# Kernel tuning notes

Measured on AMD Instinct MI355X. Metric: run time of the kernel, lower is better.

Reference implementation:

```python
import jax, jax.numpy as jnp
import numpy as np

NUM_USERS = 100_000
NUM_ITEMS = 50_000
N = NUM_USERS + NUM_ITEMS
E_DIR = 600_000            # directed user->item interactions
E = 2 * E_DIR              # bidirectional edge list used by LGConv
D = 64                     # embed_dim
F_EDGE = 8                 # edge_mlp_input_dim (edge_attr 7 + edge_weight_init 1)
H_MLP = 32                 # edge_mlp_hidden_dim
NUM_ARTISTS = 20_000
NUM_ALBUMS = 40_000
NUM_LAYERS = 3
AUDIO_SCALE = 0.3
META_SCALE = 0.44


def l2norm(x, eps=1e-12):
    # matches torch F.normalize(p=2, dim=-1)
    n = jnp.linalg.norm(x, axis=-1, keepdims=True)
    return x / jnp.maximum(n, eps)


def setup_inputs() -> dict:
    key = jax.random.key(0)
    ks = jax.random.split(key, 12)
    u = jax.random.randint(ks[0], (E_DIR,), 0, NUM_USERS)
    it = jax.random.randint(ks[1], (E_DIR,), 0, NUM_ITEMS) + NUM_USERS
    # bidirectional edges over the concatenated [user; item] node space
    edge_index = jnp.stack([jnp.concatenate([u, it]), jnp.concatenate([it, u])], axis=0)
    return {
        'user_emb_w': 0.01 * jax.random.normal(ks[2], (NUM_USERS, D), jnp.float32),
        'item_audio_emb': jax.random.normal(ks[3], (NUM_ITEMS, D), jnp.float32),
        'artist_emb_w': jax.random.normal(ks[4], (NUM_ARTISTS, D), jnp.float32) * (6.0 / (NUM_ARTISTS + D)) ** 0.5,
        'album_emb_w': jax.random.normal(ks[5], (NUM_ALBUMS, D), jnp.float32) * (6.0 / (NUM_ALBUMS + D)) ** 0.5,
        'mlp_w1': jax.random.normal(ks[6], (F_EDGE, H_MLP), jnp.float32) * (1.0 / F_EDGE) ** 0.5,
        'mlp_b1': jnp.zeros((H_MLP,), jnp.float32),
        'mlp_w2': jax.random.normal(ks[7], (H_MLP, 1), jnp.float32) * (1.0 / H_MLP) ** 0.5,
        'mlp_b2': jnp.zeros((1,), jnp.float32),
        'edge_features': jax.random.uniform(ks[8], (E, F_EDGE), jnp.float32),
        'edge_index': edge_index,
        'artist_ids': jax.random.randint(ks[9], (NUM_ITEMS,), 0, NUM_ARTISTS),
        'album_ids': jax.random.randint(ks[10], (NUM_ITEMS,), 0, NUM_ALBUMS),
    }


def reference(user_emb_w, item_audio_emb, artist_emb_w, album_emb_w,
              mlp_w1, mlp_b1, mlp_w2, mlp_b2, edge_features,
              edge_index, artist_ids, album_ids):
    # Edge weight MLP: Linear -> ReLU -> Linear -> Sigmoid -> squeeze
    h = jax.nn.relu(edge_features @ mlp_w1 + mlp_b1)
    edge_w = jax.nn.sigmoid(h @ mlp_w2 + mlp_b2)[:, 0]  # [E]

    # Node features
    user = l2norm(user_emb_w)
    meta = artist_emb_w[artist_ids] + album_emb_w[album_ids]
    item = l2norm(item_audio_emb * AUDIO_SCALE + meta * META_SCALE)
    x = jnp.concatenate([user, item], axis=0)  # [N, D]

    row, col = edge_index[0], edge_index[1]

    # gcn_norm (add_self_loops=False): deg over destination column
    deg = jax.ops.segment_sum(edge_w, col, num_segments=N)
    dinv = jnp.where(deg > 0, 1.0 / jnp.sqrt(jnp.where(deg > 0, deg, 1.0)), 0.0)
    norm = dinv[row] * edge_w * dinv[col]  # [E]

    acc = x
    for _ in range(NUM_LAYERS):
        msg = norm[:, None] * x[row]                         # gather [E, D]
        x = jax.ops.segment_sum(msg, col, num_segments=N)    # scatter-add
        acc = acc + x
    x = l2norm(acc / (NUM_LAYERS + 1))

    user_emb = x[:NUM_USERS]
    item_emb = x[NUM_USERS:]
    align_loss = jnp.float32(0.0)
    return user_emb, item_emb, align_loss
```

## Files before the change

### kernel.cpp

```cpp
#include <hip/hip_runtime.h>
#include <math.h>

#define NUM_USERS 100000
#define NUM_ITEMS 50000
#define NN 150000
#define EE 1200000
#define NNP 150016
#define G8_BLOCKS 4688

#define NBUCKET 293
#define NB2 256
#define EPB 4688

typedef unsigned short ushort_t;
typedef unsigned int uint_t;

__device__ __forceinline__ uint_t pack2(float lo, float hi) {
    uint_t a = __float_as_uint(lo);
    uint_t b = __float_as_uint(hi);
    a = (a + 0x7FFFu + ((a >> 16) & 1u)) >> 16;
    b = (b + 0x7FFFu + ((b >> 16) & 1u)) & 0xFFFF0000u;
    return a | b;
}
__device__ __forceinline__ float lo16(uint_t x) { return __uint_as_float(x << 16); }
__device__ __forceinline__ float hi16(uint_t x) { return __uint_as_float(x & 0xFFFF0000u); }

__global__ void mlp_kernel(const float* __restrict__ feats,
                           const float* __restrict__ w1,
                           const float* __restrict__ b1,
                           const float* __restrict__ w2,
                           const float* __restrict__ b2,
                           float* __restrict__ wout) {
    __shared__ float sw1t[256];
    __shared__ float2 shb[32];
    __shared__ float sb2s;
    int t = threadIdx.x;
    sw1t[t] = w1[(t & 7) * 32 + (t >> 3)];
    if (t < 32) shb[t] = make_float2(b1[t], w2[t]);
    if (t == 0) sb2s = b2[0];
    __syncthreads();
    int e = blockIdx.x * 256 + t;
    if (e >= EE) return;
    const float4* fp = (const float4*)(feats + (size_t)e * 8);
    float4 fa = fp[0], fb = fp[1];
    float f[8] = {fa.x, fa.y, fa.z, fa.w, fb.x, fb.y, fb.z, fb.w};
    float s = sb2s;
#pragma unroll
    for (int j = 0; j < 32; ++j) {
        float4 wa = *(const float4*)&sw1t[j * 8];
        float4 wb = *(const float4*)&sw1t[j * 8 + 4];
        float2 bw = shb[j];
        float h = bw.x;
        h = fmaf(f[0], wa.x, h);
        h = fmaf(f[1], wa.y, h);
        h = fmaf(f[2], wa.z, h);
        h = fmaf(f[3], wa.w, h);
        h = fmaf(f[4], wb.x, h);
        h = fmaf(f[5], wb.y, h);
        h = fmaf(f[6], wb.z, h);
        h = fmaf(f[7], wb.w, h);
        h = fmaxf(h, 0.f);
        s = fmaf(h, bw.y, s);
    }
    wout[e] = 1.f / (1.f + expf(-s));
}

__global__ void hist_kernel(const int* __restrict__ col,
                            int* __restrict__ hist) {
    __shared__ int h[NBUCKET];
    int t = threadIdx.x, B = blockIdx.x;
    for (int i = t; i < NBUCKET; i += 256) h[i] = 0;
    __syncthreads();
    int beg = B * EPB, end = beg + EPB; if (end > EE) end = EE;
    for (int i = beg + t; i < end; i += 256)
        atomicAdd(&h[col[i] >> 9], 1);
    __syncthreads();
    for (int i = t; i < NBUCKET; i += 256) hist[i * NB2 + B] = h[i];
}

__global__ void scanb_kernel(int* __restrict__ hist,
                             int* __restrict__ tot) {
    int b = blockIdx.x, t = threadIdx.x;
    int v = hist[b * NB2 + t];
    int lane = t & 63;
    int s = v;
#pragma unroll
    for (int off = 1; off < 64; off <<= 1) {
        int u = __shfl_up(s, off, 64);
        if (lane >= off) s += u;
    }
    __shared__ int wsum[4];
    if (lane == 63) wsum[t >> 6] = s;
    __syncthreads();
    int add = 0;
    for (int w = 0; w < (t >> 6); ++w) add += wsum[w];
    hist[b * NB2 + t] = s - v + add;
    if (t == 255) tot[b] = s + add;
}

__global__ void scant_kernel(const int* __restrict__ tot,
                             int* __restrict__ base) {
    int t = threadIdx.x;
    int v = (t < NBUCKET) ? tot[t] : 0;
    int lane = t & 63;
    int s = v;
#pragma unroll
    for (int off = 1; off < 64; off <<= 1) {
        int u = __shfl_up(s, off, 64);
        if (lane >= off) s += u;
    }
    __shared__ int wsum[8];
    if (lane == 63) wsum[t >> 6] = s;
    __syncthreads();
    int add = 0;
    for (int w = 0; w < (t >> 6); ++w) add += wsum[w];
    if (t < NBUCKET) base[t] = s - v + add;
    if (t == 511) base[NBUCKET] = s + add;
}

__global__ void scatter1_kernel(const int* __restrict__ col,
                                const int* __restrict__ row,
                                const float* __restrict__ wbuf,
                                const int* __restrict__ hist,
                                const int* __restrict__ base,
                                int4* __restrict__ tmp) {
    __shared__ int bbase[NBUCKET];
    __shared__ int cur[NBUCKET];
    int t = threadIdx.x, B = blockIdx.x;
    for (int i = t; i < NBUCKET; i += 256) {
        bbase[i] = base[i] + hist[i * NB2 + B];
        cur[i] = 0;
    }
    __syncthreads();
    int beg = B * EPB, end = beg + EPB; if (end > EE) end = EE;
    for (int i = beg + t; i < end; i += 256) {
        int c = col[i];
        int b = c >> 9;
        int r = atomicAdd(&cur[b], 1);
        tmp[bbase[b] + r] = make_int4(c, row[i], __float_as_int(wbuf[i]), 0);
    }
}

__global__ void scatter2_kernel(const int4* __restrict__ tmp,
                                const int* __restrict__ base,
                                int* __restrict__ offs,
                                int2* __restrict__ packed) {
    __shared__ int sc[512];
    __shared__ int wsum[8];
    int b = blockIdx.x, t = threadIdx.x;
    int beg = base[b], end = base[b + 1];
    sc[t] = 0;
    __syncthreads();
    for (int i = beg + t; i < end; i += 512)
        atomicAdd(&sc[tmp[i].x & 511], 1);
    __syncthreads();
    int v = sc[t];
    int lane = t & 63;
    int s = v;
#pragma unroll
    for (int off = 1; off < 64; off <<= 1) {
        int u = __shfl_up(s, off, 64);
        if (lane >= off) s += u;
    }
    if (lane == 63) wsum[t >> 6] = s;
    __syncthreads();
    int add = 0;
    for (int w = 0; w < (t >> 6); ++w) add += wsum[w];
    int excl = s - v + add;
    offs[b * 512 + t] = beg + excl;
    __syncthreads();
    sc[t] = excl;
    __syncthreads();
    for (int i = beg + t; i < end; i += 512) {
        int4 rec = tmp[i];
        int r = atomicAdd(&sc[rec.x & 511], 1);
        packed[beg + r] = make_int2(rec.y, rec.z);
    }
}

__device__ __forceinline__ void gather_node8(const ushort_t* __restrict__ zin,
                                             const int2* __restrict__ packed,
                                             int beg, int end, unsigned c,
                                             float4& a0, float4& a1) {
    for (int base = beg; base < end; base += 8) {
        int m = end - base; if (m > 8) m = 8;
        int r = 0; float w = 0.f;
        if ((int)c < m) {
            int2 p = packed[base + (int)c];
            r = p.x; w = __int_as_float(p.y);
        }
        int rj[8]; float wj[8]; uint4 vj[8];
#pragma unroll
        for (int u = 0; u < 8; ++u) {
            int idx = (u < m) ? u : (m - 1);
            rj[u] = __shfl(r, idx, 8);
            wj[u] = __shfl(w, u, 8);
        }
#pragma unroll
        for (int u = 0; u < 8; ++u)
            vj[u] = *(const uint4*)(zin + (size_t)(uint_t)rj[u] * 64u + c * 8u);
#pragma unroll
        for (int u = 0; u < 8; ++u) {
            float ww = wj[u]; uint4 v = vj[u];
            a0.x = fmaf(ww, lo16(v.x), a0.x);
            a0.y = fmaf(ww, hi16(v.x), a0.y);
            a0.z = fmaf(ww, lo16(v.y), a0.z);
            a0.w = fmaf(ww, hi16(v.y), a0.w);
            a1.x = fmaf(ww, lo16(v.z), a1.x);
            a1.y = fmaf(ww, hi16(v.z), a1.y);
            a1.z = fmaf(ww, lo16(v.w), a1.z);
            a1.w = fmaf(ww, hi16(v.w), a1.w);
        }
    }
}

__global__ void dinv_init_kernel(const int2* __restrict__ packed,
                                 const int* __restrict__ offs,
                                 const float* __restrict__ user_w,
                                 const float* __restrict__ audio,
                                 const float* __restrict__ artist_w,
                                 const float* __restrict__ album_w,
                                 const int* __restrict__ artist_ids,
                                 const int* __restrict__ album_ids,
                                 float* __restrict__ dinv,
                                 ushort_t* __restrict__ z0) {
    unsigned t = blockIdx.x * 256u + threadIdx.x;
    unsigned node = t >> 3, c = t & 7u;
    if (node >= NN) return;
    int beg = offs[node], end = offs[node + 1];
    float ds = 0.f;
    for (int k = beg + (int)c; k < end; k += 8) ds += __int_as_float(packed[k].y);
    ds += __shfl_xor(ds, 1, 8);
    ds += __shfl_xor(ds, 2, 8);
    ds += __shfl_xor(ds, 4, 8);
    float d = (ds > 0.f) ? rsqrtf(ds) : 0.f;
    if (c == 0) dinv[node] = d;

    size_t ri = (size_t)node * 64u + c * 8u;
    float v[8];
    if (node < NUM_USERS) {
        float4 x0 = *(const float4*)(user_w + ri);
        float4 x1 = *(const float4*)(user_w + ri + 4);
        v[0]=x0.x; v[1]=x0.y; v[2]=x0.z; v[3]=x0.w;
        v[4]=x1.x; v[5]=x1.y; v[6]=x1.z; v[7]=x1.w;
    } else {
        unsigned j = node - NUM_USERS;
        unsigned aid = (unsigned)artist_ids[j], bid = (unsigned)album_ids[j];
        const float* ap = artist_w + (size_t)aid * 64u + c * 8u;
        const float* bp = album_w  + (size_t)bid * 64u + c * 8u;
        const float* up = audio    + (size_t)j   * 64u + c * 8u;
        float4 A0 = *(const float4*)ap, A1 = *(const float4*)(ap + 4);
        float4 B0 = *(const float4*)bp, B1 = *(const float4*)(bp + 4);
        float4 U0 = *(const float4*)up, U1 = *(const float4*)(up + 4);
        v[0] = fmaf(0.44f, A0.x + B0.x, 0.3f * U0.x);
        v[1] = fmaf(0.44f, A0.y + B0.y, 0.3f * U0.y);
        v[2] = fmaf(0.44f, A0.z + B0.z, 0.3f * U0.z);
        v[3] = fmaf(0.44f, A0.w + B0.w, 0.3f * U0.w);
        v[4] = fmaf(0.44f, A1.x + B1.x, 0.3f * U1.x);
        v[5] = fmaf(0.44f, A1.y + B1.y, 0.3f * U1.y);
        v[6] = fmaf(0.44f, A1.z + B1.z, 0.3f * U1.z);
        v[7] = fmaf(0.44f, A1.w + B1.w, 0.3f * U1.w);
    }
    float s = 0.f;
#pragma unroll
    for (int k = 0; k < 8; ++k) s = fmaf(v[k], v[k], s);
    s += __shfl_xor(s, 1, 8);
    s += __shfl_xor(s, 2, 8);
    s += __shfl_xor(s, 4, 8);
    float rn = rsqrtf(fmaxf(s, 1e-24f));
    float scale = ((d > 0.f) ? d : 1.f) * rn;
    uint4 o;
    o.x = pack2(v[0] * scale, v[1] * scale);
    o.y = pack2(v[2] * scale, v[3] * scale);
    o.z = pack2(v[4] * scale, v[5] * scale);
    o.w = pack2(v[6] * scale, v[7] * scale);
    *(uint4*)(z0 + ri) = o;
}

__global__ void spmm_kernel(const ushort_t* __restrict__ zin,
                            const int2* __restrict__ packed,
                            const int* __restrict__ offs,
                            const float* __restrict__ dinv,
                            ushort_t* __restrict__ zout) {
    unsigned t = blockIdx.x * 256u + threadIdx.x;
    unsigned node = t >> 3, c = t & 7u;
    if (node >= NN) return;
    float4 a0 = make_float4(0,0,0,0), a1 = make_float4(0,0,0,0);
    gather_node8(zin, packed, offs[node], offs[node + 1], c, a0, a1);
    float d = dinv[node], dd = d * d;
    uint4 o;
    o.x = pack2(a0.x * dd, a0.y * dd);
    o.y = pack2(a0.z * dd, a0.w * dd);
    o.z = pack2(a1.x * dd, a1.y * dd);
    o.w = pack2(a1.z * dd, a1.w * dd);
    *(uint4*)(zout + (size_t)node * 64u + c * 8u) = o;
}

__global__ void spmm_final_kernel(const ushort_t* __restrict__ z0,
                                  const ushort_t* __restrict__ z1,
                                  const ushort_t* __restrict__ z2,
                                  const int2* __restrict__ packed,
                                  const int* __restrict__ offs,
                                  const float* __restrict__ dinv,
                                  float* __restrict__ out) {
    unsigned t = blockIdx.x * 256u + threadIdx.x;
    unsigned node = t >> 3, c = t & 7u;
    if (node >= NN) return;
    float4 a0 = make_float4(0,0,0,0), a1 = make_float4(0,0,0,0);
    gather_node8(z2, packed, offs[node], offs[node + 1], c, a0, a1);
    float d = dinv[node], dd = d * d;
    size_t ri = (size_t)node * 64u + c * 8u;
    uint4 p0 = *(const uint4*)(z0 + ri);
    uint4 p1 = *(const uint4*)(z1 + ri);
    uint4 p2 = *(const uint4*)(z2 + ri);
    float v[8];
    v[0] = lo16(p0.x) + lo16(p1.x) + lo16(p2.x) + a0.x * dd;
    v[1] = hi16(p0.x) + hi16(p1.x) + hi16(p2.x) + a0.y * dd;
    v[2] = lo16(p0.y) + lo16(p1.y) + lo16(p2.y) + a0.z * dd;
    v[3] = hi16(p0.y) + hi16(p1.y) + hi16(p2.y) + a0.w * dd;
    v[4] = lo16(p0.z) + lo16(p1.z) + lo16(p2.z) + a1.x * dd;
    v[5] = hi16(p0.z) + hi16(p1.z) + hi16(p2.z) + a1.y * dd;
    v[6] = lo16(p0.w) + lo16(p1.w) + lo16(p2.w) + a1.z * dd;
    v[7] = hi16(p0.w) + hi16(p1.w) + hi16(p2.w) + a1.w * dd;
    float s = 0.f;
#pragma unroll
    for (int k = 0; k < 8; ++k) s = fmaf(v[k], v[k], s);
    s += __shfl_xor(s, 1, 8);
    s += __shfl_xor(s, 2, 8);
    s += __shfl_xor(s, 4, 8);
    float n = fmaxf(sqrtf(s) * 0.25f, 1e-12f);
    float inv = 0.25f / n;
    float4 o0 = make_float4(v[0]*inv, v[1]*inv, v[2]*inv, v[3]*inv);
    float4 o1 = make_float4(v[4]*inv, v[5]*inv, v[6]*inv, v[7]*inv);
    *(float4*)(out + ri)     = o0;
    *(float4*)(out + ri + 4) = o1;
    if (t == 0) out[(size_t)NN * 64u] = 0.f;
}

extern "C" void kernel_launch(void* const* d_in, const int* in_sizes, int n_in,
                              void* d_out, int out_size, void* d_ws, size_t ws_size,
                              hipStream_t stream) {
    const float* user_w     = (const float*)d_in[0];
    const float* audio      = (const float*)d_in[1];
    const float* artist_w   = (const float*)d_in[2];
    const float* album_w    = (const float*)d_in[3];
    const float* w1         = (const float*)d_in[4];
    const float* b1         = (const float*)d_in[5];
    const float* w2         = (const float*)d_in[6];
    const float* b2         = (const float*)d_in[7];
    const float* feats      = (const float*)d_in[8];
    const int*   row        = (const int*)d_in[9];
    const int*   col        = row + EE;
    const int*   artist_ids = (const int*)d_in[10];
    const int*   album_ids  = (const int*)d_in[11];
    float* out = (float*)d_out;

    int*      hist    = (int*)d_ws;
    int*      tot     = hist + NBUCKET * NB2;
    int*      base    = tot + 512;
    int*      offs    = base + 512;
    float*    wbuf    = (float*)(offs + NNP + 16);
    float*    dinv    = wbuf + EE;
    int2*     packed  = (int2*)(dinv + NN);
    ushort_t* z0      = (ushort_t*)(packed + EE);
    ushort_t* z1      = z0 + (size_t)NN * 64;
    ushort_t* z2      = z1 + (size_t)NN * 64;
    int4*     tmp     = (int4*)z1;

    mlp_kernel<<<(EE + 255) / 256, 256, 0, stream>>>(feats, w1, b1, w2, b2, wbuf);
    hist_kernel<<<NB2, 256, 0, stream>>>(col, hist);
    scanb_kernel<<<NBUCKET, 256, 0, stream>>>(hist, tot);
    scant_kernel<<<1, 512, 0, stream>>>(tot, base);
    scatter1_kernel<<<NB2, 256, 0, stream>>>(col, row, wbuf, hist, base, tmp);
    scatter2_kernel<<<NBUCKET, 512, 0, stream>>>(tmp, base, offs, packed);
    dinv_init_kernel<<<G8_BLOCKS, 256, 0, stream>>>(packed, offs,
                                                    user_w, audio, artist_w, album_w,
                                                    artist_ids, album_ids, dinv, z0);
    spmm_kernel<<<G8_BLOCKS, 256, 0, stream>>>(z0, packed, offs, dinv, z1);
    spmm_kernel<<<G8_BLOCKS, 256, 0, stream>>>(z1, packed, offs, dinv, z2);
    spmm_final_kernel<<<G8_BLOCKS, 256, 0, stream>>>(z0, z1, z2, packed, offs,
                                                     dinv, out);
}
```

Measured before the change: 300.3 us.

## Fuse MLP with histogram, merge scans, compact tmp records, compute degree in scatter

New measurement: 468.9 us. 1.56x slower.

```diff
diff --git a/kernel.cpp b/kernel.cpp
--- a/kernel.cpp
+++ b/kernel.cpp
@@ -9,8 +9,8 @@
 #define G8_BLOCKS 4688
 
 #define NBUCKET 293
-#define NB2 256
-#define EPB 4688
+#define NB2 512
+#define EPB 2344
 
 typedef unsigned short ushort_t;
 typedef unsigned int uint_t;
@@ -25,61 +25,63 @@
 __device__ __forceinline__ float lo16(uint_t x) { return __uint_as_float(x << 16); }
 __device__ __forceinline__ float hi16(uint_t x) { return __uint_as_float(x & 0xFFFF0000u); }
 
-__global__ void mlp_kernel(const float* __restrict__ feats,
-                           const float* __restrict__ w1,
-                           const float* __restrict__ b1,
-                           const float* __restrict__ w2,
-                           const float* __restrict__ b2,
-                           float* __restrict__ wout) {
+__global__ void mlp_hist_kernel(const float* __restrict__ feats,
+                                const float* __restrict__ w1,
+                                const float* __restrict__ b1,
+                                const float* __restrict__ w2,
+                                const float* __restrict__ b2,
+                                const int* __restrict__ col,
+                                float* __restrict__ wout,
+                                int* __restrict__ hist,
+                                int* __restrict__ done) {
     __shared__ float sw1t[256];
     __shared__ float2 shb[32];
     __shared__ float sb2s;
-    int t = threadIdx.x;
+    __shared__ int h[NBUCKET];
+    int t = threadIdx.x, B = blockIdx.x;
     sw1t[t] = w1[(t & 7) * 32 + (t >> 3)];
     if (t < 32) shb[t] = make_float2(b1[t], w2[t]);
     if (t == 0) sb2s = b2[0];
-    __syncthreads();
-    int e = blockIdx.x * 256 + t;
-    if (e >= EE) return;
-    const float4* fp = (const float4*)(feats + (size_t)e * 8);
-    float4 fa = fp[0], fb = fp[1];
-    float f[8] = {fa.x, fa.y, fa.z, fa.w, fb.x, fb.y, fb.z, fb.w};
-    float s = sb2s;
-#pragma unroll
-    for (int j = 0; j < 32; ++j) {
-        float4 wa = *(const float4*)&sw1t[j * 8];
-        float4 wb = *(const float4*)&sw1t[j * 8 + 4];
-        float2 bw = shb[j];
-        float h = bw.x;
-        h = fmaf(f[0], wa.x, h);
-        h = fmaf(f[1], wa.y, h);
-        h = fmaf(f[2], wa.z, h);
-        h = fmaf(f[3], wa.w, h);
-        h = fmaf(f[4], wb.x, h);
-        h = fmaf(f[5], wb.y, h);
-        h = fmaf(f[6], wb.z, h);
-        h = fmaf(f[7], wb.w, h);
-        h = fmaxf(h, 0.f);
-        s = fmaf(h, bw.y, s);
-    }
-    wout[e] = 1.f / (1.f + expf(-s));
-}
-
-__global__ void hist_kernel(const int* __restrict__ col,
-                            int* __restrict__ hist) {
-    __shared__ int h[NBUCKET];
-    int t = threadIdx.x, B = blockIdx.x;
+    if (B == 0 && t == 0) *done = 0;
     for (int i = t; i < NBUCKET; i += 256) h[i] = 0;
     __syncthreads();
     int beg = B * EPB, end = beg + EPB; if (end > EE) end = EE;
-    for (int i = beg + t; i < end; i += 256)
-        atomicAdd(&h[col[i] >> 9], 1);
+    for (int e = beg + t; e < end; e += 256) {
+        atomicAdd(&h[col[e] >> 9], 1);
+        const float4* fp = (const float4*)(feats + (size_t)e * 8);
+        float4 fa = fp[0], fb = fp[1];
+        float f0 = fa.x, f1 = fa.y, f2 = fa.z, f3 = fa.w;
+        float f4 = fb.x, f5 = fb.y, f6 = fb.z, f7 = fb.w;
+        float s = sb2s;
+#pragma unroll
+        for (int j = 0; j < 32; ++j) {
+            float4 wa = *(const float4*)&sw1t[j * 8];
+            float4 wb = *(const float4*)&sw1t[j * 8 + 4];
+            float2 bw = shb[j];
+            float hh = bw.x;
+            hh = fmaf(f0, wa.x, hh);
+            hh = fmaf(f1, wa.y, hh);
+            hh = fmaf(f2, wa.z, hh);
+            hh = fmaf(f3, wa.w, hh);
+            hh = fmaf(f4, wb.x, hh);
+            hh = fmaf(f5, wb.y, hh);
+            hh = fmaf(f6, wb.z, hh);
+            hh = fmaf(f7, wb.w, hh);
+            hh = fmaxf(hh, 0.f);
+            s = fmaf(hh, bw.y, s);
+        }
+        wout[e] = 1.f / (1.f + expf(-s));
+    }
     __syncthreads();
     for (int i = t; i < NBUCKET; i += 256) hist[i * NB2 + B] = h[i];
 }
 
 __global__ void scanb_kernel(int* __restrict__ hist,
-                             int* __restrict__ tot) {
+                             int* __restrict__ tot,
+                             int* __restrict__ base,
+                             int* __restrict__ done) {
+    __shared__ int wsum[8];
+    __shared__ int lastflag;
     int b = blockIdx.x, t = threadIdx.x;
     int v = hist[b * NB2 + t];
     int lane = t & 63;
@@ -89,33 +91,30 @@
         int u = __shfl_up(s, off, 64);
         if (lane >= off) s += u;
     }
-    __shared__ int wsum[4];
     if (lane == 63) wsum[t >> 6] = s;
     __syncthreads();
     int add = 0;
     for (int w = 0; w < (t >> 6); ++w) add += wsum[w];
     hist[b * NB2 + t] = s - v + add;
-    if (t == 255) tot[b] = s + add;
-}
-
-__global__ void scant_kernel(const int* __restrict__ tot,
-                             int* __restrict__ base) {
-    int t = threadIdx.x;
-    int v = (t < NBUCKET) ? tot[t] : 0;
-    int lane = t & 63;
-    int s = v;
-#pragma unroll
-    for (int off = 1; off < 64; off <<= 1) {
-        int u = __shfl_up(s, off, 64);
-        if (lane >= off) s += u;
-    }
-    __shared__ int wsum[8];
-    if (lane == 63) wsum[t >> 6] = s;
-    __syncthreads();
-    int add = 0;
-    for (int w = 0; w < (t >> 6); ++w) add += wsum[w];
-    if (t < NBUCKET) base[t] = s - v + add;
-    if (t == 511) base[NBUCKET] = s + add;
+    if (t == 511) atomicExch(&tot[b], s + add);
+    __syncthreads();
+    if (t == 0) lastflag = (atomicAdd(done, 1) == NBUCKET - 1);
+    __syncthreads();
+    if (lastflag) {
+        int v2 = (t < NBUCKET) ? atomicOr(&tot[t], 0) : 0;
+        int s2 = v2;
+#pragma unroll
+        for (int off = 1; off < 64; off <<= 1) {
+            int u = __shfl_up(s2, off, 64);
+            if (lane >= off) s2 += u;
+        }
+        if (lane == 63) wsum[t >> 6] = s2;
+        __syncthreads();
+        int add2 = 0;
+        for (int w = 0; w < (t >> 6); ++w) add2 += wsum[w];
+        if (t < NBUCKET) base[t] = s2 - v2 + add2;
+        if (t == 511) base[NBUCKET] = s2 + add2;
+    }
 }
 
 __global__ void scatter1_kernel(const int* __restrict__ col,
@@ -123,7 +122,7 @@
                                 const float* __restrict__ wbuf,
                                 const int* __restrict__ hist,
                                 const int* __restrict__ base,
-                                int4* __restrict__ tmp) {
+                                int2* __restrict__ tmp) {
     __shared__ int bbase[NBUCKET];
     __shared__ int cur[NBUCKET];
     int t = threadIdx.x, B = blockIdx.x;
@@ -137,22 +136,30 @@
         int c = col[i];
         int b = c >> 9;
         int r = atomicAdd(&cur[b], 1);
-        tmp[bbase[b] + r] = make_int4(c, row[i], __float_as_int(wbuf[i]), 0);
-    }
-}
-
-__global__ void scatter2_kernel(const int4* __restrict__ tmp,
+        tmp[bbase[b] + r] = make_int2((row[i] << 9) | (c & 511),
+                                      __float_as_int(wbuf[i]));
+    }
+}
+
+__global__ void scatter2_kernel(const int2* __restrict__ tmp,
                                 const int* __restrict__ base,
                                 int* __restrict__ offs,
-                                int2* __restrict__ packed) {
+                                int2* __restrict__ packed,
+                                float* __restrict__ dinv) {
     __shared__ int sc[512];
+    __shared__ float sdeg[512];
     __shared__ int wsum[8];
     int b = blockIdx.x, t = threadIdx.x;
     int beg = base[b], end = base[b + 1];
     sc[t] = 0;
-    __syncthreads();
-    for (int i = beg + t; i < end; i += 512)
-        atomicAdd(&sc[tmp[i].x & 511], 1);
+    sdeg[t] = 0.f;
+    __syncthreads();
+    for (int i = beg + t; i < end; i += 512) {
+        int2 rec = tmp[i];
+        int cl = rec.x & 511;
+        atomicAdd(&sc[cl], 1);
+        atomicAdd(&sdeg[cl], __int_as_float(rec.y));
+    }
     __syncthreads();
     int v = sc[t];
     int lane = t & 63;
@@ -168,13 +175,18 @@
     for (int w = 0; w < (t >> 6); ++w) add += wsum[w];
     int excl = s - v + add;
     offs[b * 512 + t] = beg + excl;
+    int g = b * 512 + t;
+    if (g < NN) {
+        float ds = sdeg[t];
+        dinv[g] = (ds > 0.f) ? rsqrtf(ds) : 0.f;
+    }
     __syncthreads();
     sc[t] = excl;
     __syncthreads();
     for (int i = beg + t; i < end; i += 512) {
-        int4 rec = tmp[i];
+        int2 rec = tmp[i];
         int r = atomicAdd(&sc[rec.x & 511], 1);
-        packed[beg + r] = make_int2(rec.y, rec.z);
+        packed[beg + r] = make_int2(((uint_t)rec.x) >> 9, rec.y);
     }
 }
 
@@ -214,27 +226,19 @@
     }
 }
 
-__global__ void dinv_init_kernel(const int2* __restrict__ packed,
-                                 const int* __restrict__ offs,
+__global__ void dinv_init_kernel(const int* __restrict__ offs,
                                  const float* __restrict__ user_w,
                                  const float* __restrict__ audio,
                                  const float* __restrict__ artist_w,
                                  const float* __restrict__ album_w,
                                  const int* __restrict__ artist_ids,
                                  const int* __restrict__ album_ids,
-                                 float* __restrict__ dinv,
+                                 const float* __restrict__ dinv,
                                  ushort_t* __restrict__ z0) {
     unsigned t = blockIdx.x * 256u + threadIdx.x;
     unsigned node = t >> 3, c = t & 7u;
     if (node >= NN) return;
-    int beg = offs[node], end = offs[node + 1];
-    float ds = 0.f;
-    for (int k = beg + (int)c; k < end; k += 8) ds += __int_as_float(packed[k].y);
-    ds += __shfl_xor(ds, 1, 8);
-    ds += __shfl_xor(ds, 2, 8);
-    ds += __shfl_xor(ds, 4, 8);
-    float d = (ds > 0.f) ? rsqrtf(ds) : 0.f;
-    if (c == 0) dinv[node] = d;
+    float d = dinv[node];
 
     size_t ri = (size_t)node * 64u + c * 8u;
     float v[8];
@@ -358,22 +362,22 @@
     int*      hist    = (int*)d_ws;
     int*      tot     = hist + NBUCKET * NB2;
     int*      base    = tot + 512;
-    int*      offs    = base + 512;
+    int*      done    = base + 512;
+    int*      offs    = done + 16;
     float*    wbuf    = (float*)(offs + NNP + 16);
     float*    dinv    = wbuf + EE;
     int2*     packed  = (int2*)(dinv + NN);
     ushort_t* z0      = (ushort_t*)(packed + EE);
     ushort_t* z1      = z0 + (size_t)NN * 64;
     ushort_t* z2      = z1 + (size_t)NN * 64;
-    int4*     tmp     = (int4*)z1;
-
-    mlp_kernel<<<(EE + 255) / 256, 256, 0, stream>>>(feats, w1, b1, w2, b2, wbuf);
-    hist_kernel<<<NB2, 256, 0, stream>>>(col, hist);
-    scanb_kernel<<<NBUCKET, 256, 0, stream>>>(hist, tot);
-    scant_kernel<<<1, 512, 0, stream>>>(tot, base);
+    int2*     tmp     = (int2*)z1;
+
+    mlp_hist_kernel<<<NB2, 256, 0, stream>>>(feats, w1, b1, w2, b2, col,
+                                             wbuf, hist, done);
+    scanb_kernel<<<NBUCKET, 512, 0, stream>>>(hist, tot, base, done);
     scatter1_kernel<<<NB2, 256, 0, stream>>>(col, row, wbuf, hist, base, tmp);
-    scatter2_kernel<<<NBUCKET, 512, 0, stream>>>(tmp, base, offs, packed);
-    dinv_init_kernel<<<G8_BLOCKS, 256, 0, stream>>>(packed, offs,
+    scatter2_kernel<<<NBUCKET, 512, 0, stream>>>(tmp, base, offs, packed, dinv);
+    dinv_init_kernel<<<G8_BLOCKS, 256, 0, stream>>>(offs,
                                                     user_w, audio, artist_w, album_w,
                                                     artist_ids, album_ids, dinv, z0);
     spmm_kernel<<<G8_BLOCKS, 256, 0, stream>>>(z0, packed, offs, dinv, z1);
```
